# Kernel optimization log

Measured on AMD Instinct MI355X. Metric: run time of the kernel, lower is better.

## Reference

```python
import jax, jax.numpy as jnp
import numpy as np

B, T, DIM = 4, 1024, 2048
N_HEADS, N_KV_HEADS = 32, 8
HEAD_DIM = DIM // N_HEADS  # 64
N_REPS = N_HEADS // N_KV_HEADS  # 4


def setup_inputs() -> dict:
    key = jax.random.key(0)
    ks = jax.random.split(key, 8)
    # RoPE tables: theta = 10000^{-2i/d}, positions 0..T-1
    inv_freq = 1.0 / (10000.0 ** (jnp.arange(0, HEAD_DIM, 2, dtype=jnp.float32) / HEAD_DIM))
    angles = jnp.arange(T, dtype=jnp.float32)[:, None] * inv_freq[None, :]  # (T, HEAD_DIM//2)
    s = 0.02
    return {
        "input": jax.random.normal(ks[0], (B, T, DIM), jnp.float32),
        "freqs_cos": jnp.cos(angles),
        "freqs_sin": jnp.sin(angles),
        "mask": jnp.tril(jnp.ones((T, T), dtype=bool)),  # causal boolean mask
        "wq": s * jax.random.normal(ks[1], (DIM, DIM), jnp.float32),
        "wk": s * jax.random.normal(ks[2], (N_KV_HEADS * HEAD_DIM, DIM), jnp.float32),
        "wv": s * jax.random.normal(ks[3], (N_KV_HEADS * HEAD_DIM, DIM), jnp.float32),
        "wo": s * jax.random.normal(ks[4], (DIM, DIM), jnp.float32),
        "curr_pos": 0,
    }


def _apply_rope(x, cos, sin):
    # x: (B, T, H, D); cos/sin: (T, D//2). Complex multiply on (even, odd) pairs.
    xr = x[..., 0::2]
    xi = x[..., 1::2]
    c = cos[None, :, None, :]
    s = sin[None, :, None, :]
    out_r = xr * c - xi * s
    out_i = xr * s + xi * c
    return jnp.stack([out_r, out_i], axis=-1).reshape(x.shape)


def reference(input, freqs_cos, freqs_sin, mask, wq, wk, wv, wo, curr_pos):
    Bv, Tv = input.shape[0], input.shape[1]
    qs = (input @ wq.T).reshape(Bv, Tv, N_HEADS, HEAD_DIM)
    ks = (input @ wk.T).reshape(Bv, Tv, N_KV_HEADS, HEAD_DIM)
    vs = (input @ wv.T).reshape(Bv, Tv, N_KV_HEADS, HEAD_DIM)
    qs = _apply_rope(qs, freqs_cos, freqs_sin)
    ks = _apply_rope(ks, freqs_cos, freqs_sin)

    # KV cache (prefill path: curr_pos == 0, fresh cache of length 2T)
    kv_cache = jnp.zeros((Bv, 2 * Tv, N_KV_HEADS, HEAD_DIM, 2), input.dtype)
    kv_cache = kv_cache.at[:, curr_pos:curr_pos + Tv, :, :, 0].set(ks)
    kv_cache = kv_cache.at[:, curr_pos:curr_pos + Tv, :, :, 1].set(vs)
    k_all = kv_cache[:, :curr_pos + Tv, :, :, 0]
    v_all = kv_cache[:, :curr_pos + Tv, :, :, 1]

    # GQA: broadcast each kv head across its query-head group (avoid repeat_interleave copy)
    S = k_all.shape[1]
    q = qs.transpose(0, 2, 1, 3).reshape(Bv, N_KV_HEADS, N_REPS, Tv, HEAD_DIM)
    k = k_all.transpose(0, 2, 1, 3)  # (B, KVH, S, D)
    v = v_all.transpose(0, 2, 1, 3)

    scale = 1.0 / jnp.sqrt(jnp.asarray(HEAD_DIM, input.dtype))
    scores = jnp.einsum("bgrqd,bgkd->bgrqk", q, k) * scale  # (B, KVH, REPS, T, S)
    neg = jnp.asarray(jnp.finfo(input.dtype).min, input.dtype)
    scores = jnp.where(mask[None, None, None, :, :S], scores, neg)
    attn = jax.nn.softmax(scores, axis=-1)
    out = jnp.einsum("bgrqk,bgkd->bgrqd", attn, v)
    out = out.reshape(Bv, N_HEADS, Tv, HEAD_DIM).transpose(0, 2, 1, 3).reshape(Bv, Tv, DIM)
    return out @ wo.T
```

## Files before the change

kernel.cpp:

```cpp
#include <hip/hip_runtime.h>
#include <cstdint>

typedef __bf16 bf16x8 __attribute__((ext_vector_type(8)));
typedef float  f32x4  __attribute__((ext_vector_type(4)));
typedef float  f32x16 __attribute__((ext_vector_type(16)));
typedef float  float8v __attribute__((ext_vector_type(8)));
typedef unsigned short ushort8v __attribute__((ext_vector_type(8)));
typedef unsigned short ushort4v __attribute__((ext_vector_type(4)));
typedef unsigned int   uint4v   __attribute__((ext_vector_type(4)));

__device__ __forceinline__ unsigned short f2b(float f) {
  uint32_t u = __builtin_bit_cast(uint32_t, f);
  u += 0x7FFFu + ((u >> 16) & 1u);
  return (unsigned short)(u >> 16);
}
__device__ __forceinline__ float b2f(unsigned short h) {
  uint32_t u = ((uint32_t)h) << 16;
  return __builtin_bit_cast(float, u);
}
__device__ __forceinline__ unsigned int cvtpk(float lo, float hi_) {
  unsigned int r;
  asm("v_cvt_pk_bf16_f32 %0, %1, %2" : "=v"(r) : "v"(lo), "v"(hi_));
  return r;
}

__device__ __forceinline__ void async16(const void* g, void* l) {
  __builtin_amdgcn_global_load_lds(
      (const __attribute__((address_space(1))) void*)g,
      (__attribute__((address_space(3))) void*)l, 16, 0, 0);
}

#define WAITVM(N)  __builtin_amdgcn_s_waitcnt(0x0F70 | ((N) & 15))
#define WAITLGKM0  __builtin_amdgcn_s_waitcnt(0xC07F)

__global__ void cvt_kernel(const float* __restrict__ src, unsigned short* __restrict__ dst, long n) {
  long i = ((long)blockIdx.x * blockDim.x + threadIdx.x) * 8;
  long stride = (long)gridDim.x * blockDim.x * 8;
  for (; i < n; i += stride) {
    float8v f = *(const float8v*)(src + i);
    ushort8v o;
#pragma unroll
    for (int j = 0; j < 8; ++j) o[j] = f2b(f[j]);
    *(ushort8v*)(dst + i) = o;
  }
}

template<bool F32OUT, int BN>
__global__ __launch_bounds__(512, 1)
void gemm8p(const unsigned short* __restrict__ Ag, const unsigned short* __restrict__ Wg,
            void* __restrict__ Cp, int M, int N) {
  constexpr int K = 2048;
  constexpr int NF = BN / 64;
  constexpr int BL = BN / 128;
  constexpr int VN = 4 + 2 * BL;
  constexpr int VT1 = (BN == 256) ? 6 : 4;
  constexpr int VT2 = (BN == 256) ? 4 : 3;
  constexpr int VT3 = (BN == 256) ? 2 : 1;
  constexpr int ASLOT = 16384;
  constexpr int BSLOT = BN * 64;

  extern __shared__ char lds_c[];

  const int tid = threadIdx.x;
  const int wave = tid >> 6, lane = tid & 63;
  const int wm = wave >> 2, wn = wave & 3;
  const int lr = lane & 15, lg = lane >> 4;
  const int m0 = blockIdx.y * 256, n0 = blockIdx.x * BN;

  const int laneSw = (lr >> 1) * 128 + (((((lr & 1) << 2) | lg) ^ (lr >> 1)) << 4);
  const int aoff = wm * 8192 + laneSw;
  const int boff = wn * NF * 1024 + laneSw;

  f32x4 acc[8][NF] = {};

  auto stageHT = [&](int s) {
    const int ty = s & 3;
    const int kh = (s >> 1) & 1;
    const int buf = (s >> 2) & 1;
    const int kc = (s >> 2) * 64 + kh * 32;
    if (ty == 0 || ty == 2) {
      char* slot = lds_c + (buf * 2 + kh) * ASLOT;
#pragma unroll
      for (int j = 0; j < 2; ++j) {
        int q = (tid + 512 * j) * 16;
        int R = q >> 7, g2L = ((q >> 4) & 7) ^ (R & 7);
        int row = R * 2 + (g2L >> 2), kg = g2L & 3;
        async16(Ag + (size_t)(m0 + row) * K + kc + kg * 8, slot + q);
      }
    } else {
      char* slot = lds_c + 65536 + (buf * 2 + kh) * BSLOT;
#pragma unroll
      for (int j = 0; j < BL; ++j) {
        int q = (tid + 512 * j) * 16;
        int R = q >> 7, g2L = ((q >> 4) & 7) ^ (R & 7);
        int row = R * 2 + (g2L >> 2), kg = g2L & 3;
        async16(Wg + (size_t)(n0 + row) * K + kc + kg * 8, slot + q);
      }
    }
  };

#define PHASE(BUF, KH, MH, VM, ...)                                           \
  {                                                                           \
    const char* As_ = lds_c + ((BUF) * 2 + (KH)) * ASLOT;                     \
    const char* Bs_ = lds_c + 65536 + ((BUF) * 2 + (KH)) * BSLOT;             \
    bf16x8 af_[4], bf_[NF];                                                   \
    _Pragma("unroll") for (int mi = 0; mi < 4; ++mi)                          \
      af_[mi] = *(const bf16x8*)(As_ + aoff + (MH) * 4096 + mi * 1024);       \
    _Pragma("unroll") for (int ni = 0; ni < NF; ++ni)                         \
      bf_[ni] = *(const bf16x8*)(Bs_ + boff + ni * 1024);                     \
    __VA_ARGS__;                                                              \
    WAITVM(VM);                                                               \
    __builtin_amdgcn_s_barrier();                                             \
    WAITLGKM0;                                                                \
    __builtin_amdgcn_sched_barrier(0);                                        \
    __builtin_amdgcn_s_setprio(1);                                            \
    _Pragma("unroll") for (int mi = 0; mi < 4; ++mi)                          \
      _Pragma("unroll") for (int ni = 0; ni < NF; ++ni)                       \
        acc[(MH) * 4 + mi][ni] = __builtin_amdgcn_mfma_f32_16x16x32_bf16(     \
            af_[mi], bf_[ni], acc[(MH) * 4 + mi][ni], 0, 0, 0);               \
    __builtin_amdgcn_s_setprio(0);                                            \
    __builtin_amdgcn_s_barrier();                                             \
  }

#pragma unroll
  for (int s = 0; s < 6; ++s) stageHT(s);
  WAITVM(VN);
  __builtin_amdgcn_s_barrier();

#pragma unroll 2
  for (int kt = 0; kt < 30; ++kt) {
    const int buf = kt & 1;
    const int s0 = kt * 4 + 6;
    PHASE(buf, 0, 0, VN, stageHT(s0));
    PHASE(buf, 0, 1, VN, stageHT(s0 + 1));
    PHASE(buf, 1, 0, VN, stageHT(s0 + 2));
    PHASE(buf, 1, 1, VN, stageHT(s0 + 3));
  }
  PHASE(0, 0, 0, VN, stageHT(126));
  PHASE(0, 0, 1, VN, stageHT(127));
  PHASE(0, 1, 0, VT1, (void)0);
  PHASE(0, 1, 1, VT2, (void)0);
  PHASE(1, 0, 0, VT3, (void)0);
  PHASE(1, 0, 1, 0, (void)0);
  PHASE(1, 1, 0, 0, (void)0);
  PHASE(1, 1, 1, 0, (void)0);
#undef PHASE

#pragma unroll
  for (int mig = 0; mig < 8; ++mig) {
#pragma unroll
    for (int j = 0; j < 4; ++j) {
      int row = m0 + wm * 128 + mig * 16 + lg * 4 + j;
#pragma unroll
      for (int ni = 0; ni < NF; ++ni) {
        int col = n0 + wn * (NF * 16) + ni * 16 + lr;
        float v = acc[mig][ni][j];
        if (F32OUT) ((float*)Cp)[(size_t)row * N + col] = v;
        else        ((unsigned short*)Cp)[(size_t)row * N + col] = f2b(v);
      }
    }
  }
}

__global__ void rope_kernel(unsigned short* __restrict__ qkv,
                            const float* __restrict__ cosb, const float* __restrict__ sinb) {
  long idx = (long)blockIdx.x * blockDim.x + threadIdx.x;
  const long total = (long)4096 * 1280;
  if (idx >= total) return;
  int row = (int)(idx / 1280);
  int p   = (int)(idx % 1280);
  int col0 = (p < 1024) ? (2 * p) : (2048 + 2 * (p - 1024));
  int t  = row & 1023;
  int dp = p & 31;
  float c = cosb[t * 32 + dp], s = sinb[t * 32 + dp];
  unsigned short* base = qkv + (size_t)row * 3072 + col0;
  float x0 = b2f(base[0]), x1 = b2f(base[1]);
  base[0] = f2b(x0 * c - x1 * s);
  base[1] = f2b(x0 * s + x1 * c);
}

__global__ __launch_bounds__(256)
void vtrans_kernel(const unsigned short* __restrict__ qkv, unsigned short* __restrict__ vt) {
  const int tt0 = blockIdx.x * 64;
  const int kvh = blockIdx.y;
  const int b   = blockIdx.z;
  __shared__ unsigned short lT[64 * 68];
  const int tid = threadIdx.x;
#pragma unroll
  for (int i = 0; i < 2; ++i) {
    int r = i * 32 + (tid >> 3), c = (tid & 7) * 8;
    const unsigned short* src = qkv + (size_t)(b * 1024 + tt0 + r) * 3072 + 2560 + kvh * 64 + c;
    ushort8v v = *(const ushort8v*)src;
    ushort4v a, b4;
#pragma unroll
    for (int j = 0; j < 4; ++j) { a[j] = v[j]; b4[j] = v[j + 4]; }
    *(ushort4v*)&lT[r * 68 + c]     = a;
    *(ushort4v*)&lT[r * 68 + c + 4] = b4;
  }
  __syncthreads();
#pragma unroll
  for (int i = 0; i < 2; ++i) {
    int d = tid & 63;
    int tt = i * 4 + (tid >> 6);
    ushort8v o;
#pragma unroll
    for (int j = 0; j < 8; ++j) o[j] = lT[(tt * 8 + j) * 68 + d];
    *(ushort8v*)&vt[((size_t)((b * 8 + kvh) * 64 + d)) * 1024 + tt0 + tt * 8] = o;
  }
}

__global__ __launch_bounds__(256, 2)
void attn_kernel(const unsigned short* __restrict__ qkv, const unsigned short* __restrict__ vt,
                 unsigned short* __restrict__ ob) {
  const int bx = blockIdx.x, kvh = blockIdx.y, b = blockIdx.z;
  const int tid = threadIdx.x, wave = tid >> 6, lane = tid & 63;
  const int l31 = lane & 31, hi = lane >> 5;
  const int h = kvh * 4 + wave;

  const int qth = 31 - bx, qtl = bx;
  const int q0h = qth * 32, q0l = qtl * 32;
  const int nth = qth / 2 + 1, ntl = qtl / 2 + 1;

  __shared__ unsigned short lK[2][64 * 64];
  __shared__ unsigned short lVt[2][64 * 64];

  bf16x8 qfh[4], qfl[4];
  {
    const unsigned short* qph = qkv + (size_t)(b * 1024 + q0h + l31) * 3072 + h * 64;
    const unsigned short* qpl = qkv + (size_t)(b * 1024 + q0l + l31) * 3072 + h * 64;
#pragma unroll
    for (int dk = 0; dk < 4; ++dk) {
      qfh[dk] = *(const bf16x8*)(qph + dk * 16 + hi * 8);
      qfl[dk] = *(const bf16x8*)(qpl + dk * 16 + hi * 8);
    }
  }

  f32x16 oh[2] = {}, ol[2] = {};
  float mh = -3e38f, lh = 0.f, ml = -3e38f, ll = 0.f;

  const unsigned short* kg = qkv + (size_t)(b * 1024) * 3072 + 2048 + kvh * 64;
  const unsigned short* vg = vt + (size_t)(b * 8 + kvh) * 64 * 1024;

  const int sr  = tid >> 3;
  const int scb = (tid & 7) * 16;

  auto stage = [&](int it, int bi) {
    const int kvb = it * 64;
#pragma unroll
    for (int i = 0; i < 2; ++i) {
      int r = i * 32 + sr;
      int cb = scb ^ ((r & 7) << 4);
      async16(kg + (size_t)(kvb + r) * 3072 + (cb >> 1), &lK[bi][r * 64 + (scb >> 1)]);
      async16(vg + (size_t)r * 1024 + kvb + (cb >> 1), &lVt[bi][r * 64 + (scb >> 1)]);
    }
  };

  const float SC = 0.125f * 1.44269504f;
  auto softmax = [&](f32x16 (&sd)[2], float& m2, float& l_run, f32x16 (&oacc)[2],
                     int q0, bool last, int kvb, bf16x8 (&pfrag)[2][2]) {
#pragma unroll
    for (int s = 0; s < 2; ++s)
#pragma unroll
      for (int r = 0; r < 16; ++r) {
        float v = sd[s][r] * SC;
        if (last) {
          int kvg = kvb + s * 32 + (r & 3) + 8 * (r >> 2) + 4 * hi;
          if (kvg > q0 + l31) v = -3e38f;
        }
        sd[s][r] = v;
      }
    float pm = sd[0][0];
#pragma unroll
    for (int s = 0; s < 2; ++s)
#pragma unroll
      for (int r = 0; r < 16; ++r) pm = fmaxf(pm, sd[s][r]);
    pm = fmaxf(pm, __shfl_xor(pm, 32));
    if (!__all(pm <= m2 + 11.0f)) {
      float mnew = fmaxf(m2, pm);
      float alpha = exp2f(m2 - mnew);
      m2 = mnew;
      l_run *= alpha;
#pragma unroll
      for (int db = 0; db < 2; ++db)
#pragma unroll
        for (int r = 0; r < 16; ++r) oacc[db][r] *= alpha;
    }
    float tsum = 0.f;
#pragma unroll
    for (int s = 0; s < 2; ++s)
#pragma unroll
      for (int r = 0; r < 16; ++r) { float p = exp2f(sd[s][r] - m2); sd[s][r] = p; tsum += p; }
    tsum += __shfl_xor(tsum, 32);
    l_run += tsum;
#pragma unroll
    for (int s = 0; s < 2; ++s)
#pragma unroll
      for (int kc = 0; kc < 2; ++kc) {
        unsigned int cA = cvtpk(sd[s][8 * kc + 0], sd[s][8 * kc + 1]);
        unsigned int cB = cvtpk(sd[s][8 * kc + 4], sd[s][8 * kc + 5]);
        unsigned int cC = cvtpk(sd[s][8 * kc + 2], sd[s][8 * kc + 3]);
        unsigned int cD = cvtpk(sd[s][8 * kc + 6], sd[s][8 * kc + 7]);
        unsigned int xA = __shfl_xor(cA, 32), xB = __shfl_xor(cB, 32);
        unsigned int xC = __shfl_xor(cC, 32), xD = __shfl_xor(cD, 32);
        uint4v u;
        u[0] = hi ? xB : cA;
        u[1] = hi ? xD : cC;
        u[2] = hi ? cB : xA;
        u[3] = hi ? cD : xC;
        pfrag[s][kc] = __builtin_bit_cast(bf16x8, u);
      }
  };

  stage(0, 0);
  __syncthreads();

  for (int it = 0; it < nth; ++it) {
    const int cur = it & 1;
    if (it + 1 < nth) stage(it + 1, cur ^ 1);
    const bool lo_on = (it < ntl);
    const int kvb = it * 64;

    f32x16 sh[2] = {}, sl[2] = {};
    __builtin_amdgcn_s_setprio(1);
#pragma unroll
    for (int s = 0; s < 2; ++s) {
      const int krow = s * 32 + l31;
      const char* kr = (const char*)lK[cur] + krow * 128;
      const int swz = (krow & 7) << 4;
#pragma unroll
      for (int dk = 0; dk < 4; ++dk) {
        bf16x8 kf = *(const bf16x8*)(kr + ((dk * 32 + hi * 16) ^ swz));
        sh[s] = __builtin_amdgcn_mfma_f32_32x32x16_bf16(kf, qfh[dk], sh[s], 0, 0, 0);
      }
    }
    if (lo_on) {
#pragma unroll
      for (int s = 0; s < 2; ++s) {
        const int krow = s * 32 + l31;
        const char* kr = (const char*)lK[cur] + krow * 128;
        const int swz = (krow & 7) << 4;
#pragma unroll
        for (int dk = 0; dk < 4; ++dk) {
          bf16x8 kf = *(const bf16x8*)(kr + ((dk * 32 + hi * 16) ^ swz));
          sl[s] = __builtin_amdgcn_mfma_f32_32x32x16_bf16(kf, qfl[dk], sl[s], 0, 0, 0);
        }
      }
    }
    __builtin_amdgcn_s_setprio(0);

    bf16x8 pfh[2][2], pfl[2][2];
    softmax(sh, mh, lh, oh, q0h, it == nth - 1, kvb, pfh);
    if (lo_on) softmax(sl, ml, ll, ol, q0l, it == ntl - 1, kvb, pfl);

    __builtin_amdgcn_s_setprio(1);
#pragma unroll
    for (int db = 0; db < 2; ++db) {
      const char* vr = (const char*)lVt[cur] + (db * 32 + l31) * 128;
      const int vswz = (l31 & 7) << 4;
#pragma unroll
      for (int s = 0; s < 2; ++s)
#pragma unroll
        for (int kc = 0; kc < 2; ++kc) {
          bf16x8 vf = *(const bf16x8*)(vr + ((s * 64 + kc * 32 + hi * 16) ^ vswz));
          oh[db] = __builtin_amdgcn_mfma_f32_32x32x16_bf16(vf, pfh[s][kc], oh[db], 0, 0, 0);
        }
    }
    if (lo_on) {
#pragma unroll
      for (int db = 0; db < 2; ++db) {
        const char* vr = (const char*)lVt[cur] + (db * 32 + l31) * 128;
        const int vswz = (l31 & 7) << 4;
#pragma unroll
        for (int s = 0; s < 2; ++s)
#pragma unroll
          for (int kc = 0; kc < 2; ++kc) {
            bf16x8 vf = *(const bf16x8*)(vr + ((s * 64 + kc * 32 + hi * 16) ^ vswz));
            ol[db] = __builtin_amdgcn_mfma_f32_32x32x16_bf16(vf, pfl[s][kc], ol[db], 0, 0, 0);
          }
      }
    }
    __builtin_amdgcn_s_setprio(0);

    __syncthreads();
  }

  {
    float inv = 1.0f / lh;
    unsigned short* orow = ob + (size_t)(b * 1024 + q0h + l31) * 2048 + h * 64;
#pragma unroll
    for (int db = 0; db < 2; ++db)
#pragma unroll
      for (int g = 0; g < 4; ++g) {
        int d0 = db * 32 + 8 * g + 4 * hi;
        ushort4v o;
#pragma unroll
        for (int j = 0; j < 4; ++j) o[j] = f2b(oh[db][4 * g + j] * inv);
        *(ushort4v*)(orow + d0) = o;
      }
  }
  {
    float inv = 1.0f / ll;
    unsigned short* orow = ob + (size_t)(b * 1024 + q0l + l31) * 2048 + h * 64;
#pragma unroll
    for (int db = 0; db < 2; ++db)
#pragma unroll
      for (int g = 0; g < 4; ++g) {
        int d0 = db * 32 + 8 * g + 4 * hi;
        ushort4v o;
#pragma unroll
        for (int j = 0; j < 4; ++j) o[j] = f2b(ol[db][4 * g + j] * inv);
        *(ushort4v*)(orow + d0) = o;
      }
  }
}

extern "C" void kernel_launch(void* const* d_in, const int* in_sizes, int n_in,
                              void* d_out, int out_size, void* d_ws, size_t ws_size,
                              hipStream_t stream) {
  const float* input = (const float*)d_in[0];
  const float* fcos  = (const float*)d_in[1];
  const float* fsin  = (const float*)d_in[2];
  const float* wq = (const float*)d_in[4];
  const float* wk = (const float*)d_in[5];
  const float* wv = (const float*)d_in[6];
  const float* wo = (const float*)d_in[7];
  float* out = (float*)d_out;

  unsigned short* xb   = (unsigned short*)d_ws;
  unsigned short* wqkv = xb + (size_t)4096 * 2048;
  unsigned short* wob  = wqkv + (size_t)3072 * 2048;
  unsigned short* qkv  = wob + (size_t)2048 * 2048;
  unsigned short* ob   = qkv + (size_t)4096 * 3072;
  unsigned short* vtb  = xb;

  hipFuncSetAttribute((const void*)&gemm8p<false, 256>,
                      hipFuncAttributeMaxDynamicSharedMemorySize, 131072);
  hipFuncSetAttribute((const void*)&gemm8p<true, 128>,
                      hipFuncAttributeMaxDynamicSharedMemorySize, 98304);

  auto cvt = [&](const float* s, unsigned short* d, long n) {
    long nb = (n / 8 + 255) / 256;
    int blocks = (int)(nb > 2048 ? 2048 : nb);
    hipLaunchKernelGGL(cvt_kernel, dim3(blocks), dim3(256), 0, stream, s, d, n);
  };
  cvt(input, xb, (long)4096 * 2048);
  cvt(wq, wqkv,                         (long)2048 * 2048);
  cvt(wk, wqkv + (size_t)2048 * 2048,   (long)512 * 2048);
  cvt(wv, wqkv + (size_t)2560 * 2048,   (long)512 * 2048);
  cvt(wo, wob,                          (long)2048 * 2048);

  hipLaunchKernelGGL((gemm8p<false, 256>), dim3(3072 / 256, 4096 / 256), dim3(512), 131072,
                     stream, xb, wqkv, (void*)qkv, 4096, 3072);

  hipLaunchKernelGGL(rope_kernel, dim3((4096 * 1280) / 256), dim3(256), 0, stream,
                     qkv, fcos, fsin);

  hipLaunchKernelGGL(vtrans_kernel, dim3(16, 8, 4), dim3(256), 0, stream, qkv, vtb);

  hipLaunchKernelGGL(attn_kernel, dim3(16, 8, 4), dim3(256), 0, stream, qkv, vtb, ob);

  hipLaunchKernelGGL((gemm8p<true, 128>), dim3(2048 / 128, 4096 / 256), dim3(512), 98304,
                     stream, ob, wob, (void*)out, 4096, 2048);
}
```

Measured before the change: 187.1 us.

## Fuse conversions and RoPE passes, enlarge attention KV tile, swizzle block order

```diff
diff --git a/kernel.cpp b/kernel.cpp
--- a/kernel.cpp
+++ b/kernel.cpp
@@ -33,19 +33,30 @@
 #define WAITVM(N)  __builtin_amdgcn_s_waitcnt(0x0F70 | ((N) & 15))
 #define WAITLGKM0  __builtin_amdgcn_s_waitcnt(0xC07F)
 
-__global__ void cvt_kernel(const float* __restrict__ src, unsigned short* __restrict__ dst, long n) {
-  long i = ((long)blockIdx.x * blockDim.x + threadIdx.x) * 8;
-  long stride = (long)gridDim.x * blockDim.x * 8;
-  for (; i < n; i += stride) {
-    float8v f = *(const float8v*)(src + i);
-    ushort8v o;
-#pragma unroll
-    for (int j = 0; j < 8; ++j) o[j] = f2b(f[j]);
-    *(ushort8v*)(dst + i) = o;
-  }
-}
-
-template<bool F32OUT, int BN>
+struct CvtArgs {
+  const float* src[5];
+  unsigned short* dst[5];
+  long n[5];
+};
+__global__ void cvt5_kernel(CvtArgs a) {
+  long base = (long)blockIdx.x * blockDim.x + threadIdx.x;
+  long gstride = (long)gridDim.x * blockDim.x;
+#pragma unroll 1
+  for (int sg = 0; sg < 5; ++sg) {
+    const float* s = a.src[sg];
+    unsigned short* d = a.dst[sg];
+    long n8 = a.n[sg] >> 3;
+    for (long i = base; i < n8; i += gstride) {
+      float8v f = *(const float8v*)(s + i * 8);
+      ushort8v o;
+#pragma unroll
+      for (int j = 0; j < 8; ++j) o[j] = f2b(f[j]);
+      *(ushort8v*)(d + i * 8) = o;
+    }
+  }
+}
+
+template<bool F32OUT, int BN, int GX>
 __global__ __launch_bounds__(512, 1)
 void gemm8p(const unsigned short* __restrict__ Ag, const unsigned short* __restrict__ Wg,
             void* __restrict__ Cp, int M, int N) {
@@ -58,6 +69,7 @@
   constexpr int VT3 = (BN == 256) ? 2 : 1;
   constexpr int ASLOT = 16384;
   constexpr int BSLOT = BN * 64;
+  constexpr int CPX = 2 * GX;
 
   extern __shared__ char lds_c[];
 
@@ -65,7 +77,10 @@
   const int wave = tid >> 6, lane = tid & 63;
   const int wm = wave >> 2, wn = wave & 3;
   const int lr = lane & 15, lg = lane >> 4;
-  const int m0 = blockIdx.y * 256, n0 = blockIdx.x * BN;
+
+  const int flat = blockIdx.y * GX + blockIdx.x;
+  const int swz = (flat & 7) * CPX + (flat >> 3);
+  const int m0 = (swz / GX) * 256, n0 = (swz % GX) * BN;
 
   const int laneSw = (lr >> 1) * 128 + (((((lr & 1) << 2) | lg) ^ (lr >> 1)) << 4);
   const int aoff = wm * 8192 + laneSw;
@@ -162,30 +177,43 @@
   }
 }
 
-__global__ void rope_kernel(unsigned short* __restrict__ qkv,
-                            const float* __restrict__ cosb, const float* __restrict__ sinb) {
-  long idx = (long)blockIdx.x * blockDim.x + threadIdx.x;
-  const long total = (long)4096 * 1280;
-  if (idx >= total) return;
-  int row = (int)(idx / 1280);
-  int p   = (int)(idx % 1280);
-  int col0 = (p < 1024) ? (2 * p) : (2048 + 2 * (p - 1024));
-  int t  = row & 1023;
-  int dp = p & 31;
-  float c = cosb[t * 32 + dp], s = sinb[t * 32 + dp];
-  unsigned short* base = qkv + (size_t)row * 3072 + col0;
-  float x0 = b2f(base[0]), x1 = b2f(base[1]);
-  base[0] = f2b(x0 * c - x1 * s);
-  base[1] = f2b(x0 * s + x1 * c);
-}
-
 __global__ __launch_bounds__(256)
-void vtrans_kernel(const unsigned short* __restrict__ qkv, unsigned short* __restrict__ vt) {
+void ropekv_kernel(unsigned short* __restrict__ qkv,
+                   const float* __restrict__ cosb, const float* __restrict__ sinb,
+                   unsigned short* __restrict__ vt) {
   const int tt0 = blockIdx.x * 64;
   const int kvh = blockIdx.y;
   const int b   = blockIdx.z;
+  const int tid = threadIdx.x;
+
+  {
+    int r = tid >> 2, c0 = (tid & 3) * 16;
+    int t = tt0 + r;
+    unsigned short* kp = qkv + (size_t)(b * 1024 + t) * 3072 + 2048 + kvh * 64 + c0;
+    const float* cb = cosb + t * 32 + c0 / 2;
+    const float* sb = sinb + t * 32 + c0 / 2;
+    ushort8v x0 = *(const ushort8v*)kp;
+    ushort8v x1 = *(const ushort8v*)(kp + 8);
+    float8v c = *(const float8v*)cb;
+    float8v s = *(const float8v*)sb;
+    ushort8v o0, o1;
+#pragma unroll
+    for (int j = 0; j < 4; ++j) {
+      float xr = b2f(x0[2 * j]), xi = b2f(x0[2 * j + 1]);
+      o0[2 * j]     = f2b(xr * c[j] - xi * s[j]);
+      o0[2 * j + 1] = f2b(xr * s[j] + xi * c[j]);
+    }
+#pragma unroll
+    for (int j = 0; j < 4; ++j) {
+      float xr = b2f(x1[2 * j]), xi = b2f(x1[2 * j + 1]);
+      o1[2 * j]     = f2b(xr * c[4 + j] - xi * s[4 + j]);
+      o1[2 * j + 1] = f2b(xr * s[4 + j] + xi * c[4 + j]);
+    }
+    *(ushort8v*)kp = o0;
+    *(ushort8v*)(kp + 8) = o1;
+  }
+
   __shared__ unsigned short lT[64 * 68];
-  const int tid = threadIdx.x;
 #pragma unroll
   for (int i = 0; i < 2; ++i) {
     int r = i * 32 + (tid >> 3), c = (tid & 7) * 8;
@@ -211,28 +239,45 @@
 
 __global__ __launch_bounds__(256, 2)
 void attn_kernel(const unsigned short* __restrict__ qkv, const unsigned short* __restrict__ vt,
+                 const float* __restrict__ cosb, const float* __restrict__ sinb,
                  unsigned short* __restrict__ ob) {
-  const int bx = blockIdx.x, kvh = blockIdx.y, b = blockIdx.z;
+  const int flat = (blockIdx.z * 8 + blockIdx.y) * 16 + blockIdx.x;
+  const int swzb = (flat & 7) * 64 + (flat >> 3);
+  const int bx = swzb & 15, kvh = (swzb >> 4) & 7, b = swzb >> 7;
+
   const int tid = threadIdx.x, wave = tid >> 6, lane = tid & 63;
   const int l31 = lane & 31, hi = lane >> 5;
   const int h = kvh * 4 + wave;
 
   const int qth = 31 - bx, qtl = bx;
   const int q0h = qth * 32, q0l = qtl * 32;
-  const int nth = qth / 2 + 1, ntl = qtl / 2 + 1;
-
-  __shared__ unsigned short lK[2][64 * 64];
-  __shared__ unsigned short lVt[2][64 * 64];
+  const int nth = qth / 4 + 1, ntl = qtl / 4 + 1;
+
+  __shared__ unsigned short lK[2][128 * 64];
+  __shared__ unsigned short lVt[2][64 * 128];
 
   bf16x8 qfh[4], qfl[4];
   {
-    const unsigned short* qph = qkv + (size_t)(b * 1024 + q0h + l31) * 3072 + h * 64;
-    const unsigned short* qpl = qkv + (size_t)(b * 1024 + q0l + l31) * 3072 + h * 64;
-#pragma unroll
-    for (int dk = 0; dk < 4; ++dk) {
-      qfh[dk] = *(const bf16x8*)(qph + dk * 16 + hi * 8);
-      qfl[dk] = *(const bf16x8*)(qpl + dk * 16 + hi * 8);
-    }
+    auto ldq = [&](int q0, bf16x8* qf) {
+      int t = q0 + l31;
+      const unsigned short* qp = qkv + (size_t)(b * 1024 + t) * 3072 + h * 64;
+#pragma unroll
+      for (int dk = 0; dk < 4; ++dk) {
+        ushort8v q = *(const ushort8v*)(qp + dk * 16 + hi * 8);
+        f32x4 c4 = *(const f32x4*)(cosb + t * 32 + dk * 8 + hi * 4);
+        f32x4 s4 = *(const f32x4*)(sinb + t * 32 + dk * 8 + hi * 4);
+        ushort8v o;
+#pragma unroll
+        for (int j = 0; j < 4; ++j) {
+          float xr = b2f(q[2 * j]), xi = b2f(q[2 * j + 1]);
+          o[2 * j]     = f2b(xr * c4[j] - xi * s4[j]);
+          o[2 * j + 1] = f2b(xr * s4[j] + xi * c4[j]);
+        }
+        qf[dk] = __builtin_bit_cast(bf16x8, o);
+      }
+    };
+    ldq(q0h, qfh);
+    ldq(q0l, qfl);
   }
 
   f32x16 oh[2] = {}, ol[2] = {};
@@ -241,25 +286,46 @@
   const unsigned short* kg = qkv + (size_t)(b * 1024) * 3072 + 2048 + kvh * 64;
   const unsigned short* vg = vt + (size_t)(b * 8 + kvh) * 64 * 1024;
 
-  const int sr  = tid >> 3;
-  const int scb = (tid & 7) * 16;
-
   auto stage = [&](int it, int bi) {
-    const int kvb = it * 64;
-#pragma unroll
-    for (int i = 0; i < 2; ++i) {
+    const int kvb = it * 128;
+    const int sr  = tid >> 3;
+    const int scb = (tid & 7) * 16;
+#pragma unroll
+    for (int i = 0; i < 4; ++i) {
       int r = i * 32 + sr;
       int cb = scb ^ ((r & 7) << 4);
       async16(kg + (size_t)(kvb + r) * 3072 + (cb >> 1), &lK[bi][r * 64 + (scb >> 1)]);
-      async16(vg + (size_t)r * 1024 + kvb + (cb >> 1), &lVt[bi][r * 64 + (scb >> 1)]);
+    }
+    const int rv0 = tid >> 4;
+    const int scv = (tid & 15) * 16;
+#pragma unroll
+    for (int i = 0; i < 4; ++i) {
+      int rv = i * 16 + rv0;
+      int cbv = scv ^ ((rv & 15) << 4);
+      async16(vg + (size_t)rv * 1024 + kvb + (cbv >> 1), &lVt[bi][rv * 128 + (scv >> 1)]);
     }
   };
 
   const float SC = 0.125f * 1.44269504f;
-  auto softmax = [&](f32x16 (&sd)[2], float& m2, float& l_run, f32x16 (&oacc)[2],
-                     int q0, bool last, int kvb, bf16x8 (&pfrag)[2][2]) {
-#pragma unroll
-    for (int s = 0; s < 2; ++s)
+  auto state = [&](int cur, int kvb, bf16x8 (&qf)[4], float& m2, float& l_run,
+                   f32x16 (&oacc)[2], int q0, bool last) {
+    f32x16 sd[4] = {};
+    __builtin_amdgcn_s_setprio(1);
+#pragma unroll
+    for (int s = 0; s < 4; ++s) {
+      const int krow = s * 32 + l31;
+      const char* kr = (const char*)lK[cur] + krow * 128;
+      const int swz = (krow & 7) << 4;
+#pragma unroll
+      for (int dk = 0; dk < 4; ++dk) {
+        bf16x8 kf = *(const bf16x8*)(kr + ((dk * 32 + hi * 16) ^ swz));
+        sd[s] = __builtin_amdgcn_mfma_f32_32x32x16_bf16(kf, qf[dk], sd[s], 0, 0, 0);
+      }
+    }
+    __builtin_amdgcn_s_setprio(0);
+
+#pragma unroll
+    for (int s = 0; s < 4; ++s)
 #pragma unroll
       for (int r = 0; r < 16; ++r) {
         float v = sd[s][r] * SC;
@@ -271,7 +337,7 @@
       }
     float pm = sd[0][0];
 #pragma unroll
-    for (int s = 0; s < 2; ++s)
+    for (int s = 0; s < 4; ++s)
 #pragma unroll
       for (int r = 0; r < 16; ++r) pm = fmaxf(pm, sd[s][r]);
     pm = fmaxf(pm, __shfl_xor(pm, 32));
@@ -287,13 +353,15 @@
     }
     float tsum = 0.f;
 #pragma unroll
-    for (int s = 0; s < 2; ++s)
+    for (int s = 0; s < 4; ++s)
 #pragma unroll
       for (int r = 0; r < 16; ++r) { float p = exp2f(sd[s][r] - m2); sd[s][r] = p; tsum += p; }
     tsum += __shfl_xor(tsum, 32);
     l_run += tsum;
-#pragma unroll
-    for (int s = 0; s < 2; ++s)
+
+    bf16x8 pf[4][2];
+#pragma unroll
+    for (int s = 0; s < 4; ++s)
 #pragma unroll
       for (int kc = 0; kc < 2; ++kc) {
         unsigned int cA = cvtpk(sd[s][8 * kc + 0], sd[s][8 * kc + 1]);
@@ -307,8 +375,24 @@
         u[1] = hi ? xD : cC;
         u[2] = hi ? cB : xA;
         u[3] = hi ? cD : xC;
-        pfrag[s][kc] = __builtin_bit_cast(bf16x8, u);
-      }
+        pf[s][kc] = __builtin_bit_cast(bf16x8, u);
+      }
+
+    __builtin_amdgcn_s_setprio(1);
+#pragma unroll
+    for (int db = 0; db < 2; ++db) {
+      const int row = db * 32 + l31;
+      const char* vr = (const char*)lVt[cur] + row * 256;
+      const int vswz = (row & 15) << 4;
+#pragma unroll
+      for (int s = 0; s < 4; ++s)
+#pragma unroll
+        for (int kc = 0; kc < 2; ++kc) {
+          bf16x8 vf = *(const bf16x8*)(vr + ((s * 64 + kc * 32 + hi * 16) ^ vswz));
+          oacc[db] = __builtin_amdgcn_mfma_f32_32x32x16_bf16(vf, pf[s][kc], oacc[db], 0, 0, 0);
+        }
+    }
+    __builtin_amdgcn_s_setprio(0);
   };
 
   stage(0, 0);
@@ -317,69 +401,10 @@
   for (int it = 0; it < nth; ++it) {
     const int cur = it & 1;
     if (it + 1 < nth) stage(it + 1, cur ^ 1);
-    const bool lo_on = (it < ntl);
-    const int kvb = it * 64;
-
-    f32x16 sh[2] = {}, sl[2] = {};
-    __builtin_amdgcn_s_setprio(1);
-#pragma unroll
-    for (int s = 0; s < 2; ++s) {
-      const int krow = s * 32 + l31;
-      const char* kr = (const char*)lK[cur] + krow * 128;
-      const int swz = (krow & 7) << 4;
-#pragma unroll
-      for (int dk = 0; dk < 4; ++dk) {
-        bf16x8 kf = *(const bf16x8*)(kr + ((dk * 32 + hi * 16) ^ swz));
-        sh[s] = __builtin_amdgcn_mfma_f32_32x32x16_bf16(kf, qfh[dk], sh[s], 0, 0, 0);
-      }
-    }
-    if (lo_on) {
-#pragma unroll
-      for (int s = 0; s < 2; ++s) {
-        const int krow = s * 32 + l31;
-        const char* kr = (const char*)lK[cur] + krow * 128;
-        const int swz = (krow & 7) << 4;
-#pragma unroll
-        for (int dk = 0; dk < 4; ++dk) {
-          bf16x8 kf = *(const bf16x8*)(kr + ((dk * 32 + hi * 16) ^ swz));
-          sl[s] = __builtin_amdgcn_mfma_f32_32x32x16_bf16(kf, qfl[dk], sl[s], 0, 0, 0);
-        }
-      }
-    }
-    __builtin_amdgcn_s_setprio(0);
-
-    bf16x8 pfh[2][2], pfl[2][2];
-    softmax(sh, mh, lh, oh, q0h, it == nth - 1, kvb, pfh);
-    if (lo_on) softmax(sl, ml, ll, ol, q0l, it == ntl - 1, kvb, pfl);
-
-    __builtin_amdgcn_s_setprio(1);
-#pragma unroll
-    for (int db = 0; db < 2; ++db) {
-      const char* vr = (const char*)lVt[cur] + (db * 32 + l31) * 128;
-      const int vswz = (l31 & 7) << 4;
-#pragma unroll
-      for (int s = 0; s < 2; ++s)
-#pragma unroll
-        for (int kc = 0; kc < 2; ++kc) {
-          bf16x8 vf = *(const bf16x8*)(vr + ((s * 64 + kc * 32 + hi * 16) ^ vswz));
-          oh[db] = __builtin_amdgcn_mfma_f32_32x32x16_bf16(vf, pfh[s][kc], oh[db], 0, 0, 0);
-        }
-    }
-    if (lo_on) {
-#pragma unroll
-      for (int db = 0; db < 2; ++db) {
-        const char* vr = (const char*)lVt[cur] + (db * 32 + l31) * 128;
-        const int vswz = (l31 & 7) << 4;
-#pragma unroll
-        for (int s = 0; s < 2; ++s)
-#pragma unroll
-          for (int kc = 0; kc < 2; ++kc) {
-            bf16x8 vf = *(const bf16x8*)(vr + ((s * 64 + kc * 32 + hi * 16) ^ vswz));
-            ol[db] = __builtin_amdgcn_mfma_f32_32x32x16_bf16(vf, pfl[s][kc], ol[db], 0, 0, 0);
-          }
-      }
-    }
-    __builtin_amdgcn_s_setprio(0);
+    const int kvb = it * 128;
+
+    state(cur, kvb, qfh, mh, lh, oh, q0h, it == nth - 1);
+    if (it < ntl) state(cur, kvb, qfl, ml, ll, ol, q0l, it == ntl - 1);
 
     __syncthreads();
   }
@@ -433,32 +458,28 @@
   unsigned short* ob   = qkv + (size_t)4096 * 3072;
   unsigned short* vtb  = xb;
 
-  hipFuncSetAttribute((const void*)&gemm8p<false, 256>,
+  hipFuncSetAttribute((const void*)&gemm8p<false, 256, 12>,
                       hipFuncAttributeMaxDynamicSharedMemorySize, 131072);
-  hipFuncSetAttribute((const void*)&gemm8p<true, 128>,
+  hipFuncSetAttribute((const void*)&gemm8p<true, 128, 16>,
                       hipFuncAttributeMaxDynamicSharedMemorySize, 98304);
 
-  auto cvt = [&](const float* s, unsigned short* d, long n) {
-    long nb = (n / 8 + 255) / 256;
-    int blocks = (int)(nb > 2048 ? 2048 : nb);
-    hipLaunchKernelGGL(cvt_kernel, dim3(blocks), dim3(256), 0, stream, s, d, n);
-  };
-  cvt(input, xb, (long)4096 * 2048);
-  cvt(wq, wqkv,                         (long)2048 * 2048);
-  cvt(wk, wqkv + (size_t)2048 * 2048,   (long)512 * 2048);
-  cvt(wv, wqkv + (size_t)2560 * 2048,   (long)512 * 2048);
-  cvt(wo, wob,                          (long)2048 * 2048);
-
-  hipLaunchKernelGGL((gemm8p<false, 256>), dim3(3072 / 256, 4096 / 256), dim3(512), 131072,
+  CvtArgs ca;
+  ca.src[0] = input; ca.dst[0] = xb;                        ca.n[0] = (long)4096 * 2048;
+  ca.src[1] = wq;    ca.dst[1] = wqkv;                      ca.n[1] = (long)2048 * 2048;
+  ca.src[2] = wk;    ca.dst[2] = wqkv + (size_t)2048 * 2048; ca.n[2] = (long)512 * 2048;
+  ca.src[3] = wv;    ca.dst[3] = wqkv + (size_t)2560 * 2048; ca.n[3] = (long)512 * 2048;
+  ca.src[4] = wo;    ca.dst[4] = wob;                       ca.n[4] = (long)2048 * 2048;
+  hipLaunchKernelGGL(cvt5_kernel, dim3(2048), dim3(256), 0, stream, ca);
+
+  hipLaunchKernelGGL((gemm8p<false, 256, 12>), dim3(12, 16), dim3(512), 131072,
                      stream, xb, wqkv, (void*)qkv, 4096, 3072);
 
-  hipLaunchKernelGGL(rope_kernel, dim3((4096 * 1280) / 256), dim3(256), 0, stream,
-                     qkv, fcos, fsin);
-
-  hipLaunchKernelGGL(vtrans_kernel, dim3(16, 8, 4), dim3(256), 0, stream, qkv, vtb);
-
-  hipLaunchKernelGGL(attn_kernel, dim3(16, 8, 4), dim3(256), 0, stream, qkv, vtb, ob);
-
-  hipLaunchKernelGGL((gemm8p<true, 128>), dim3(2048 / 128, 4096 / 256), dim3(512), 98304,
+  hipLaunchKernelGGL(ropekv_kernel, dim3(16, 8, 4), dim3(256), 0, stream,
+                     qkv, fcos, fsin, vtb);
+
+  hipLaunchKernelGGL(attn_kernel, dim3(16, 8, 4), dim3(256), 0, stream,
+                     qkv, vtb, fcos, fsin, ob);
+
+  hipLaunchKernelGGL((gemm8p<true, 128, 16>), dim3(16, 16), dim3(512), 98304,
                      stream, ob, wob, (void*)out, 4096, 2048);
 }
```

Result: no change. 185.3 us (-1.0%).
